# Optimization experiments

Measured on AMD Instinct MI355X. Metric: run time of the kernel, lower is better.

## Reference

```python
import jax, jax.numpy as jnp
import numpy as np

B, S, H, NH = 4, 320, 512, 8
DH = H // NH
RAND_S = 320  # weibo randomAttention size
NEG = -1e15


def setup_inputs() -> dict:
    rng = jax.random.key(0)
    ks = jax.random.split(rng, 14)
    s = 0.02
    return {
        "query": jax.random.normal(ks[0], (B, S, H), jnp.float32),
        "key": jax.random.normal(ks[1], (B, S, H), jnp.float32),
        "value": jax.random.normal(ks[2], (B, S, H), jnp.float32),
        "rel_pos_embedding": jax.random.normal(ks[3], (B, S, S, H), jnp.float32),
        "seq_len": jax.random.randint(ks[4], (B,), 1, S + 1),
        "lex_num": 0,
        "Wq": jax.random.normal(ks[5], (H, H), jnp.float32) * s,
        "bq": jax.random.normal(ks[6], (H,), jnp.float32) * s,
        "Wv": jax.random.normal(ks[7], (H, H), jnp.float32) * s,
        "bv": jax.random.normal(ks[8], (H,), jnp.float32) * s,
        "Wr": jax.random.normal(ks[9], (H, H), jnp.float32) * s,
        "br": jax.random.normal(ks[10], (H,), jnp.float32) * s,
        "u": jax.random.normal(ks[11], (NH, DH), jnp.float32) * s,
        "v": jax.random.normal(ks[12], (NH, DH), jnp.float32) * s,
        "rand_attn": jax.random.normal(ks[13], (1, NH, RAND_S, RAND_S), jnp.float32) * s,
    }


def reference(query, key, value, rel_pos_embedding, seq_len, lex_num,
              Wq, bq, Wv, bv, Wr, br, u, v, rand_attn):
    # Linear projections (torch Linear: x @ W.T + b). Note: key is NOT projected.
    q = query @ Wq.T + bq                      # [B,S,H]
    val = value @ Wv.T + bv                    # [B,S,H]
    rel = rel_pos_embedding @ Wr.T + br        # [B,S,S,H]

    # Split heads
    q = q.reshape(B, S, NH, DH).transpose(0, 2, 1, 3)     # [B,NH,S,DH]
    k = key.reshape(B, S, NH, DH).transpose(0, 2, 1, 3)   # [B,NH,S,DH]
    val = val.reshape(B, S, NH, DH).transpose(0, 2, 1, 3) # [B,NH,S,DH]
    rel = rel.reshape(B, S, S, NH, DH)                    # [B,Sq,Sk,NH,DH]

    # A+C: (q + u) k^T
    A_C = jnp.einsum('bhqd,bhkd->bhqk', q + u[None, :, None, :], k)
    # B+D: (q + v) contracted with relative position embeddings
    B_D = jnp.einsum('bhqd,bqkhd->bhqk', q + v[None, :, None, :], rel)

    scores = A_C + B_D + rand_attn[:, :, :S, :S]          # [B,NH,S,S]

    lengths = seq_len + lex_num                           # [B]
    mask = jnp.arange(S)[None, :] < lengths[:, None]      # [B,S] key mask
    scores = jnp.where(mask[:, None, None, :], scores, NEG)

    attn = jax.nn.softmax(scores, axis=-1)                # dropout p=0 -> identity
    out = jnp.einsum('bhqk,bhkd->bhqd', attn, val)        # [B,NH,S,DH]
    return out.transpose(0, 2, 1, 3).reshape(B, S, H)
```

## Files before the change

kernel.cpp:

```cpp
#include <hip/hip_runtime.h>


#define NEGV (-1e15f)

typedef unsigned int u32;

__device__ __forceinline__ void gl_lds16(const float* g, float* l) {
  __builtin_amdgcn_global_load_lds(
      (const __attribute__((address_space(1))) u32*)(g),
      (__attribute__((address_space(3))) u32*)(l), 16, 0, 0);
}

__device__ __forceinline__ float dot4f(const float4 a, const float4 b) {
  return a.x*b.x + a.y*b.y + a.z*b.z + a.w*b.w;
}

__global__ __launch_bounds__(256) void k1_proj(
    const float* __restrict__ query, const float* __restrict__ value,
    const float* __restrict__ Wq, const float* __restrict__ bq,
    const float* __restrict__ Wv, const float* __restrict__ bv,
    const float* __restrict__ u, const float* __restrict__ v,
    float* __restrict__ qu, float* __restrict__ qv, float* __restrict__ valp)
{
  const int rt = blockIdx.x;
  const int ct = blockIdx.y;
  const int which = blockIdx.z;
  const int t = threadIdx.x;
  const int R0 = rt * 16;

  __shared__ float xs[16][516];

  const float* X = which ? value : query;
  const float* W = which ? Wv : Wq;
  const float* bias = which ? bv : bq;

  #pragma unroll
  for (int j = 0; j < 8; ++j) {
    int f4 = t + 256 * j;
    int row = f4 >> 7, c4 = f4 & 127;
    float4 xv = *reinterpret_cast<const float4*>(X + (size_t)(R0 + row) * 512 + c4 * 4);
    *reinterpret_cast<float4*>(&xs[row][c4 * 4]) = xv;
  }
  __syncthreads();

  const int r = t >> 4, clo = t & 15;
  #pragma unroll
  for (int sub = 0; sub < 2; ++sub) {
    const int cb = ct * 128 + sub * 64 + clo * 4;
    float a0 = 0.f, a1 = 0.f, a2 = 0.f, a3 = 0.f;
    const float* w0p = W + (size_t)(cb + 0) * 512;
    const float* w1p = W + (size_t)(cb + 1) * 512;
    const float* w2p = W + (size_t)(cb + 2) * 512;
    const float* w3p = W + (size_t)(cb + 3) * 512;
    #pragma unroll 2
    for (int m4 = 0; m4 < 128; ++m4) {
      float4 x4 = *reinterpret_cast<const float4*>(&xs[r][m4 * 4]);
      float4 w0 = *reinterpret_cast<const float4*>(w0p + m4 * 4);
      float4 w1 = *reinterpret_cast<const float4*>(w1p + m4 * 4);
      float4 w2 = *reinterpret_cast<const float4*>(w2p + m4 * 4);
      float4 w3 = *reinterpret_cast<const float4*>(w3p + m4 * 4);
      a0 += dot4f(x4, w0);
      a1 += dot4f(x4, w1);
      a2 += dot4f(x4, w2);
      a3 += dot4f(x4, w3);
    }
    a0 += bias[cb + 0]; a1 += bias[cb + 1]; a2 += bias[cb + 2]; a3 += bias[cb + 3];
    const size_t ob = (size_t)(R0 + r) * 512 + cb;
    if (which == 0) {
      float4 o1, o2;
      o1.x = a0 + u[cb + 0]; o1.y = a1 + u[cb + 1]; o1.z = a2 + u[cb + 2]; o1.w = a3 + u[cb + 3];
      o2.x = a0 + v[cb + 0]; o2.y = a1 + v[cb + 1]; o2.z = a2 + v[cb + 2]; o2.w = a3 + v[cb + 3];
      *reinterpret_cast<float4*>(qu + ob) = o1;
      *reinterpret_cast<float4*>(qv + ob) = o2;
    } else {
      float4 o; o.x = a0; o.y = a1; o.z = a2; o.w = a3;
      *reinterpret_cast<float4*>(valp + ob) = o;
    }
  }
}

__global__ __launch_bounds__(256) void k2_w(
    const float* __restrict__ qv, const float* __restrict__ Wr, const float* __restrict__ br,
    float* __restrict__ w_ws, float* __restrict__ c_ws)
{
  const int rt = blockIdx.x;
  const int h  = blockIdx.y;
  const int t = threadIdx.x;
  const int R0 = rt * 16;

  __shared__ float qs[16][68];
  {
    int row = t >> 4, d4 = t & 15;
    float4 x = *reinterpret_cast<const float4*>(qv + (size_t)(R0 + row) * 512 + h * 64 + d4 * 4);
    *reinterpret_cast<float4*>(&qs[row][d4 * 4]) = x;
  }
  __syncthreads();

  const int r = t >> 4, clo = t & 15;
  #pragma unroll
  for (int sub = 0; sub < 8; ++sub) {
    const int eb = sub * 64 + clo * 4;
    float4 acc; acc.x = 0.f; acc.y = 0.f; acc.z = 0.f; acc.w = 0.f;
    #pragma unroll 4
    for (int d = 0; d < 64; ++d) {
      float s = qs[r][d];
      float4 w4 = *reinterpret_cast<const float4*>(Wr + (size_t)(h * 64 + d) * 512 + eb);
      acc.x += s * w4.x; acc.y += s * w4.y; acc.z += s * w4.z; acc.w += s * w4.w;
    }
    *reinterpret_cast<float4*>(w_ws + (size_t)(R0 + r) * 4096 + h * 512 + eb) = acc;
  }
  if (t < 16) {
    float cs = 0.f;
    for (int d = 0; d < 64; ++d) cs += qs[t][d] * br[h * 64 + d];
    c_ws[(size_t)(R0 + t) * 8 + h] = cs;
  }
}

__global__ __launch_bounds__(256, 2) void k4_attn(
    const float* __restrict__ rpe, const float* __restrict__ key,
    const float* __restrict__ rand_attn,
    const int* __restrict__ seq_len, const int* __restrict__ lex_num,
    const float* __restrict__ qu, const float* __restrict__ w_ws,
    const float* __restrict__ c_ws, const float* __restrict__ valp,
    float* __restrict__ out)
{
  const int q = blockIdx.x;
  const int b = blockIdx.y;
  const int t = threadIdx.x;
  const int wv = t >> 6, ln = t & 63;
  const int m = t & 31;
  const int r = t >> 5;

  __shared__ float bufA[2][8][512];
  __shared__ float bufB[2][8][512];
  __shared__ float sc[8][320];
  __shared__ float cl[8];

  const size_t bq512 = ((size_t)b * 320 + q) * 512;
  const float* rpe_bq = rpe + ((size_t)b * 320 + q) * 320 * 512;
  const float* key_b  = key + (size_t)b * 320 * 512;

  {
    #pragma unroll
    for (int jj = 0; jj < 4; ++jj) {
      const int chunk = jj * 256 + wv * 64;
      gl_lds16(rpe_bq + (size_t)(chunk + ln) * 4, &bufA[0][0][0] + chunk * 4);
      gl_lds16(key_b  + (size_t)(chunk + ln) * 4, &bufB[0][0][0] + chunk * 4);
    }
  }

  if (t < 8) cl[t] = c_ws[((size_t)b * 320 + q) * 8 + t];
  const int len = seq_len[b] + lex_num[0];

  float4 wwc[4][8];
  float4 quc[4];
  const float* wbase = w_ws + ((size_t)b * 320 + q) * 4096;
  #pragma unroll
  for (int j = 0; j < 4; ++j) {
    const int p4 = 4 * (m + 32 * j);
    quc[j] = *reinterpret_cast<const float4*>(qu + bq512 + p4);
    #pragma unroll
    for (int h = 0; h < 8; ++h)
      wwc[j][h] = *reinterpret_cast<const float4*>(wbase + h * 512 + p4);
  }
  __syncthreads();

  for (int h = 0; h < 8; ++h) {
    for (int k = t; k < 320; k += 256) {
      float rv = rand_attn[((size_t)h * 320 + q) * 320 + k];
      sc[h][k] = (k < len) ? rv + cl[h] : NEGV;
    }
  }
  __syncthreads();

  int cbuf = 0;
  for (int tile = 0; tile < 40; ++tile) {
    if (tile + 1 < 40) {
      const float* gA = rpe_bq + (size_t)(tile + 1) * 8 * 512;
      const float* gB = key_b  + (size_t)(tile + 1) * 8 * 512;
      const int nb = cbuf ^ 1;
      #pragma unroll
      for (int jj = 0; jj < 4; ++jj) {
        const int chunk = jj * 256 + wv * 64;
        gl_lds16(gA + (size_t)(chunk + ln) * 4, &bufA[nb][0][0] + chunk * 4);
        gl_lds16(gB + (size_t)(chunk + ln) * 4, &bufB[nb][0][0] + chunk * 4);
      }
    }

    float acc[8] = {0.f,0.f,0.f,0.f,0.f,0.f,0.f,0.f};
    float aac[4];
    #pragma unroll
    for (int j = 0; j < 4; ++j) {
      const int p4 = 4 * (m + 32 * j);
      const float4 r4 = *reinterpret_cast<const float4*>(&bufA[cbuf][r][p4]);
      const float4 k4 = *reinterpret_cast<const float4*>(&bufB[cbuf][r][p4]);
      #pragma unroll
      for (int h = 0; h < 8; ++h) acc[h] += dot4f(r4, wwc[j][h]);
      aac[j] = dot4f(k4, quc[j]);
    }

    #pragma unroll
    for (int h = 0; h < 8; ++h) {
      float vv = acc[h];
      vv += __shfl_xor(vv, 1, 32);
      vv += __shfl_xor(vv, 2, 32);
      vv += __shfl_xor(vv, 4, 32);
      vv += __shfl_xor(vv, 8, 32);
      vv += __shfl_xor(vv, 16, 32);
      acc[h] = vv;
    }
    #pragma unroll
    for (int j = 0; j < 4; ++j) {
      float vv = aac[j];
      vv += __shfl_xor(vv, 1, 16);
      vv += __shfl_xor(vv, 2, 16);
      vv += __shfl_xor(vv, 4, 16);
      vv += __shfl_xor(vv, 8, 16);
      float ov = __shfl_xor(vv, 16, 32);
      float lowv  = (m < 16) ? vv : ov;
      float highv = (m < 16) ? ov : vv;
      acc[2 * j]     += lowv;
      acc[2 * j + 1] += highv;
    }

    const int kk = tile * 8 + r;
    if (m == 0) {
      #pragma unroll
      for (int h = 0; h < 8; ++h) sc[h][kk] += acc[h];
    }
    __syncthreads();
    cbuf ^= 1;
  }

  {
    const int h = t >> 5;
    float vals[10];
    float mx = -3.0e38f;
    #pragma unroll
    for (int i = 0; i < 10; ++i) { vals[i] = sc[h][m + 32 * i]; mx = fmaxf(mx, vals[i]); }
    mx = fmaxf(mx, __shfl_xor(mx, 1, 32));
    mx = fmaxf(mx, __shfl_xor(mx, 2, 32));
    mx = fmaxf(mx, __shfl_xor(mx, 4, 32));
    mx = fmaxf(mx, __shfl_xor(mx, 8, 32));
    mx = fmaxf(mx, __shfl_xor(mx, 16, 32));
    float s = 0.f;
    #pragma unroll
    for (int i = 0; i < 10; ++i) { vals[i] = __expf(vals[i] - mx); s += vals[i]; }
    s += __shfl_xor(s, 1, 32);
    s += __shfl_xor(s, 2, 32);
    s += __shfl_xor(s, 4, 32);
    s += __shfl_xor(s, 8, 32);
    s += __shfl_xor(s, 16, 32);
    const float inv = 1.0f / s;
    #pragma unroll
    for (int i = 0; i < 10; ++i) sc[h][m + 32 * i] = vals[i] * inv;
  }
  __syncthreads();

  {
    const int h = t >> 5, d2 = m;
    float2 a0; a0.x = 0.f; a0.y = 0.f;
    float2 a1; a1.x = 0.f; a1.y = 0.f;
    const float* vb = valp + (size_t)b * 320 * 512 + h * 64 + d2 * 2;
    #pragma unroll 4
    for (int k = 0; k < 320; k += 2) {
      float p0 = sc[h][k], p1 = sc[h][k + 1];
      float2 v0 = *reinterpret_cast<const float2*>(vb + (size_t)k * 512);
      float2 v1 = *reinterpret_cast<const float2*>(vb + (size_t)(k + 1) * 512);
      a0.x += p0 * v0.x; a0.y += p0 * v0.y;
      a1.x += p1 * v1.x; a1.y += p1 * v1.y;
    }
    float2 o; o.x = a0.x + a1.x; o.y = a0.y + a1.y;
    *reinterpret_cast<float2*>(out + bq512 + h * 64 + d2 * 2) = o;
  }
}

extern "C" void kernel_launch(void* const* d_in, const int* in_sizes, int n_in,
                              void* d_out, int out_size, void* d_ws, size_t ws_size,
                              hipStream_t stream) {
  const float* query = (const float*)d_in[0];
  const float* key   = (const float*)d_in[1];
  const float* value = (const float*)d_in[2];
  const float* rpe   = (const float*)d_in[3];
  const int*   seq_len = (const int*)d_in[4];
  const int*   lex_num = (const int*)d_in[5];
  const float* Wq = (const float*)d_in[6];
  const float* bq = (const float*)d_in[7];
  const float* Wv = (const float*)d_in[8];
  const float* bv = (const float*)d_in[9];
  const float* Wr = (const float*)d_in[10];
  const float* br = (const float*)d_in[11];
  const float* u  = (const float*)d_in[12];
  const float* v  = (const float*)d_in[13];
  const float* rnd = (const float*)d_in[14];

  float* out = (float*)d_out;
  float* ws = (float*)d_ws;
  float* qu   = ws;
  float* qv   = ws + 655360;
  float* valp = ws + 1310720;
  float* w_ws = ws + 1966080;
  float* c_ws = ws + 7208960;

  k1_proj<<<dim3(80, 4, 2), 256, 0, stream>>>(query, value, Wq, bq, Wv, bv, u, v, qu, qv, valp);
  k2_w<<<dim3(80, 8), 256, 0, stream>>>(qv, Wr, br, w_ws, c_ws);
  k4_attn<<<dim3(320, 4), 256, 0, stream>>>(rpe, key, rnd, seq_len, lex_num, qu, w_ws, c_ws, valp, out);
}
```

Baseline: 797.3 us.

## Split A+C score term into separate kernel and restructure rpe streaming in attention

After: 688.6 us. 1.16x faster.

```diff
diff --git a/kernel.cpp b/kernel.cpp
--- a/kernel.cpp
+++ b/kernel.cpp
@@ -116,124 +116,143 @@
   }
 }
 
+__global__ __launch_bounds__(320) void k3_ac(
+    const float* __restrict__ qu, const float* __restrict__ key,
+    const float* __restrict__ rand_attn, const float* __restrict__ c_ws,
+    float* __restrict__ sc_ws)
+{
+  const int qt = blockIdx.x;
+  const int h  = blockIdx.y;
+  const int b  = blockIdx.z;
+  const int t  = threadIdx.x;
+  const int q0 = qt * 16;
+
+  const float* kr = key + ((size_t)b * 320 + t) * 512 + h * 64;
+  float4 krow[16];
+  #pragma unroll
+  for (int i = 0; i < 16; ++i) krow[i] = *reinterpret_cast<const float4*>(kr + i * 4);
+
+  float acc[16];
+  #pragma unroll
+  for (int qi = 0; qi < 16; ++qi) {
+    const float* qrow = qu + ((size_t)b * 320 + q0 + qi) * 512 + h * 64;
+    float a = 0.f;
+    #pragma unroll
+    for (int i = 0; i < 16; ++i) {
+      float4 q4 = *reinterpret_cast<const float4*>(qrow + i * 4);
+      a += dot4f(q4, krow[i]);
+    }
+    acc[qi] = a;
+  }
+  #pragma unroll
+  for (int qi = 0; qi < 16; ++qi) {
+    const int q = q0 + qi;
+    float r = rand_attn[((size_t)h * 320 + q) * 320 + t];
+    float c = c_ws[((size_t)b * 320 + q) * 8 + h];
+    sc_ws[(((size_t)b * 320 + q) * 8 + h) * 320 + t] = acc[qi] + r + c;
+  }
+}
+
 __global__ __launch_bounds__(256, 2) void k4_attn(
-    const float* __restrict__ rpe, const float* __restrict__ key,
-    const float* __restrict__ rand_attn,
+    const float* __restrict__ rpe,
     const int* __restrict__ seq_len, const int* __restrict__ lex_num,
-    const float* __restrict__ qu, const float* __restrict__ w_ws,
-    const float* __restrict__ c_ws, const float* __restrict__ valp,
+    const float* __restrict__ w_ws, const float* __restrict__ sc_ws,
+    const float* __restrict__ valp,
     float* __restrict__ out)
 {
   const int q = blockIdx.x;
   const int b = blockIdx.y;
   const int t = threadIdx.x;
-  const int wv = t >> 6, ln = t & 63;
-  const int m = t & 31;
-  const int r = t >> 5;
-
-  __shared__ float bufA[2][8][512];
-  __shared__ float bufB[2][8][512];
+  const int w = t >> 6;
+  const int lane = t & 63;
+  const int row8 = lane >> 3;
+  const int chunk = lane & 7;
+  const int rc = (row8 ^ chunk) & 7;
+
+  __shared__ float bufA[2][16][512];
   __shared__ float sc[8][320];
-  __shared__ float cl[8];
-
-  const size_t bq512 = ((size_t)b * 320 + q) * 512;
-  const float* rpe_bq = rpe + ((size_t)b * 320 + q) * 320 * 512;
-  const float* key_b  = key + (size_t)b * 320 * 512;
-
-  {
-    #pragma unroll
-    for (int jj = 0; jj < 4; ++jj) {
-      const int chunk = jj * 256 + wv * 64;
-      gl_lds16(rpe_bq + (size_t)(chunk + ln) * 4, &bufA[0][0][0] + chunk * 4);
-      gl_lds16(key_b  + (size_t)(chunk + ln) * 4, &bufB[0][0][0] + chunk * 4);
-    }
-  }
-
-  if (t < 8) cl[t] = c_ws[((size_t)b * 320 + q) * 8 + t];
+
+  const size_t bq = (size_t)b * 320 + q;
+  const float* rpe_bq = rpe + bq * 320 * 512;
+
+  int g[8];
+  #pragma unroll
+  for (int j = 0; j < 8; ++j) {
+    int o = (w * 8 + j) * 1024 + lane * 16;
+    int row = o >> 11;
+    int ch  = (o >> 8) & 7;
+    int win = (o >> 7) & 1;
+    int slot = (o >> 4) & 7;
+    int i = win * 8 + (slot ^ ((row ^ ch) & 7));
+    g[j] = row * 512 + (ch * 16 + i) * 4;
+  }
+
+  #pragma unroll
+  for (int j = 0; j < 8; ++j)
+    gl_lds16(rpe_bq + g[j], &bufA[0][0][0] + (w * 8 + j) * 256);
+
+  const int h0 = 2 * w, h1 = 2 * w + 1;
+  const float* wb0 = w_ws + bq * 4096 + (size_t)h0 * 512 + chunk * 64;
+  const float* wb1 = w_ws + bq * 4096 + (size_t)h1 * 512 + chunk * 64;
+  float4 wc0[16], wc1[16];
+  #pragma unroll
+  for (int i = 0; i < 16; ++i) {
+    wc0[i] = *reinterpret_cast<const float4*>(wb0 + i * 4);
+    wc1[i] = *reinterpret_cast<const float4*>(wb1 + i * 4);
+  }
+
   const int len = seq_len[b] + lex_num[0];
-
-  float4 wwc[4][8];
-  float4 quc[4];
-  const float* wbase = w_ws + ((size_t)b * 320 + q) * 4096;
-  #pragma unroll
-  for (int j = 0; j < 4; ++j) {
-    const int p4 = 4 * (m + 32 * j);
-    quc[j] = *reinterpret_cast<const float4*>(qu + bq512 + p4);
-    #pragma unroll
-    for (int h = 0; h < 8; ++h)
-      wwc[j][h] = *reinterpret_cast<const float4*>(wbase + h * 512 + p4);
-  }
-  __syncthreads();
-
+  const float* scb = sc_ws + bq * 8 * 320;
   for (int h = 0; h < 8; ++h) {
     for (int k = t; k < 320; k += 256) {
-      float rv = rand_attn[((size_t)h * 320 + q) * 320 + k];
-      sc[h][k] = (k < len) ? rv + cl[h] : NEGV;
+      float vv = scb[h * 320 + k];
+      sc[h][k] = (k < len) ? vv : NEGV;
     }
   }
   __syncthreads();
 
-  int cbuf = 0;
-  for (int tile = 0; tile < 40; ++tile) {
-    if (tile + 1 < 40) {
-      const float* gA = rpe_bq + (size_t)(tile + 1) * 8 * 512;
-      const float* gB = key_b  + (size_t)(tile + 1) * 8 * 512;
-      const int nb = cbuf ^ 1;
+  const int Cb0 = row8 * 2048 + chunk * 256 + rc * 16;
+  const char* bufbase = reinterpret_cast<const char*>(&bufA[0][0][0]);
+
+  int cb = 0;
+  for (int tile = 0; tile < 20; ++tile) {
+    if (tile + 1 < 20) {
+      const float* src = rpe_bq + (size_t)(tile + 1) * 8192;
+      float* dst = &bufA[cb ^ 1][0][0];
       #pragma unroll
-      for (int jj = 0; jj < 4; ++jj) {
-        const int chunk = jj * 256 + wv * 64;
-        gl_lds16(gA + (size_t)(chunk + ln) * 4, &bufA[nb][0][0] + chunk * 4);
-        gl_lds16(gB + (size_t)(chunk + ln) * 4, &bufB[nb][0][0] + chunk * 4);
+      for (int j = 0; j < 8; ++j)
+        gl_lds16(src + g[j], dst + (w * 8 + j) * 256);
+    }
+
+    const char* bufc = bufbase + cb * 32768;
+    #pragma unroll
+    for (int pass = 0; pass < 2; ++pass) {
+      const int C = Cb0 + pass * 16384;
+      float a0 = 0.f, a1 = 0.f;
+      #pragma unroll
+      for (int i = 0; i < 16; ++i) {
+        const float4 r4 = *reinterpret_cast<const float4*>(bufc + (C ^ (i << 4)));
+        a0 += dot4f(r4, wc0[i]);
+        a1 += dot4f(r4, wc1[i]);
       }
-    }
-
-    float acc[8] = {0.f,0.f,0.f,0.f,0.f,0.f,0.f,0.f};
-    float aac[4];
-    #pragma unroll
-    for (int j = 0; j < 4; ++j) {
-      const int p4 = 4 * (m + 32 * j);
-      const float4 r4 = *reinterpret_cast<const float4*>(&bufA[cbuf][r][p4]);
-      const float4 k4 = *reinterpret_cast<const float4*>(&bufB[cbuf][r][p4]);
-      #pragma unroll
-      for (int h = 0; h < 8; ++h) acc[h] += dot4f(r4, wwc[j][h]);
-      aac[j] = dot4f(k4, quc[j]);
-    }
-
-    #pragma unroll
-    for (int h = 0; h < 8; ++h) {
-      float vv = acc[h];
-      vv += __shfl_xor(vv, 1, 32);
-      vv += __shfl_xor(vv, 2, 32);
-      vv += __shfl_xor(vv, 4, 32);
-      vv += __shfl_xor(vv, 8, 32);
-      vv += __shfl_xor(vv, 16, 32);
-      acc[h] = vv;
-    }
-    #pragma unroll
-    for (int j = 0; j < 4; ++j) {
-      float vv = aac[j];
-      vv += __shfl_xor(vv, 1, 16);
-      vv += __shfl_xor(vv, 2, 16);
-      vv += __shfl_xor(vv, 4, 16);
-      vv += __shfl_xor(vv, 8, 16);
-      float ov = __shfl_xor(vv, 16, 32);
-      float lowv  = (m < 16) ? vv : ov;
-      float highv = (m < 16) ? ov : vv;
-      acc[2 * j]     += lowv;
-      acc[2 * j + 1] += highv;
-    }
-
-    const int kk = tile * 8 + r;
-    if (m == 0) {
-      #pragma unroll
-      for (int h = 0; h < 8; ++h) sc[h][kk] += acc[h];
+      a0 += __shfl_xor(a0, 1, 8);
+      a0 += __shfl_xor(a0, 2, 8);
+      a0 += __shfl_xor(a0, 4, 8);
+      a1 += __shfl_xor(a1, 1, 8);
+      a1 += __shfl_xor(a1, 2, 8);
+      a1 += __shfl_xor(a1, 4, 8);
+      if (chunk == 0) {
+        const int kk = tile * 16 + pass * 8 + row8;
+        sc[h0][kk] += a0;
+        sc[h1][kk] += a1;
+      }
     }
     __syncthreads();
-    cbuf ^= 1;
+    cb ^= 1;
   }
 
   {
-    const int h = t >> 5;
+    const int h = t >> 5, m = t & 31;
     float vals[10];
     float mx = -3.0e38f;
     #pragma unroll
@@ -258,7 +277,7 @@
   __syncthreads();
 
   {
-    const int h = t >> 5, d2 = m;
+    const int h = t >> 5, d2 = t & 31;
     float2 a0; a0.x = 0.f; a0.y = 0.f;
     float2 a1; a1.x = 0.f; a1.y = 0.f;
     const float* vb = valp + (size_t)b * 320 * 512 + h * 64 + d2 * 2;
@@ -271,7 +290,7 @@
       a1.x += p1 * v1.x; a1.y += p1 * v1.y;
     }
     float2 o; o.x = a0.x + a1.x; o.y = a0.y + a1.y;
-    *reinterpret_cast<float2*>(out + bq512 + h * 64 + d2 * 2) = o;
+    *reinterpret_cast<float2*>(out + bq * 512 + h * 64 + d2 * 2) = o;
   }
 }
 
@@ -296,13 +315,15 @@
 
   float* out = (float*)d_out;
   float* ws = (float*)d_ws;
-  float* qu   = ws;
-  float* qv   = ws + 655360;
-  float* valp = ws + 1310720;
-  float* w_ws = ws + 1966080;
-  float* c_ws = ws + 7208960;
+  float* qu    = ws;
+  float* qv    = ws + 655360;
+  float* valp  = ws + 1310720;
+  float* w_ws  = ws + 1966080;
+  float* c_ws  = ws + 7208960;
+  float* sc_ws = ws + 7219200;
 
   k1_proj<<<dim3(80, 4, 2), 256, 0, stream>>>(query, value, Wq, bq, Wv, bv, u, v, qu, qv, valp);
   k2_w<<<dim3(80, 8), 256, 0, stream>>>(qv, Wr, br, w_ws, c_ws);
-  k4_attn<<<dim3(320, 4), 256, 0, stream>>>(rpe, key, rnd, seq_len, lex_num, qu, w_ws, c_ws, valp, out);
-}
+  k3_ac<<<dim3(20, 8, 4), 320, 0, stream>>>(qu, key, rnd, c_ws, sc_ws);
+  k4_attn<<<dim3(320, 4), 256, 0, stream>>>(rpe, seq_len, lex_num, w_ws, sc_ws, valp, out);
+}
```
